# Optimization experiments

Measured on AMD Instinct MI355X. Metric: run time of the kernel, lower is better.

The kernel has to match this reference:

```python
import jax, jax.numpy as jnp
import numpy as np

NEG_SLOPE = 0.2
N_NODES = 51200      # batch 256 graphs x 200 nodes
NODE_PER_G = 200
IN_DIM = 200
HID = 64
HEADS = 4
N_CLASSES = 2
E_RAND = 16 * N_NODES


def setup_inputs() -> dict:
    key = jax.random.key(0)
    ks = jax.random.split(key, 12)
    feat = jax.random.normal(ks[0], (N_NODES, IN_DIM), dtype=jnp.float32)
    # random edges kept within each 200-node graph block + self-loops (no zero in-degree)
    g_off = (jnp.arange(E_RAND) % (N_NODES // NODE_PER_G)) * NODE_PER_G
    src = jax.random.randint(ks[1], (E_RAND,), 0, NODE_PER_G) + g_off
    dst = jax.random.randint(ks[2], (E_RAND,), 0, NODE_PER_G) + g_off
    loop = jnp.arange(N_NODES)
    src = jnp.concatenate([src, loop]).astype(jnp.int32)
    dst = jnp.concatenate([dst, loop]).astype(jnp.int32)
    s = 0.05
    W0 = jax.random.normal(ks[3], (IN_DIM, HEADS * HID), dtype=jnp.float32) * s
    al0 = jax.random.normal(ks[4], (HEADS, HID), dtype=jnp.float32) * s
    ar0 = jax.random.normal(ks[5], (HEADS, HID), dtype=jnp.float32) * s
    W1 = jax.random.normal(ks[6], (HEADS * HID, HEADS * HID), dtype=jnp.float32) * s
    al1 = jax.random.normal(ks[7], (HEADS, HID), dtype=jnp.float32) * s
    ar1 = jax.random.normal(ks[8], (HEADS, HID), dtype=jnp.float32) * s
    Wc = jax.random.normal(ks[9], (NODE_PER_G * HID, N_CLASSES), dtype=jnp.float32) * s
    bc = jnp.zeros((N_CLASSES,), dtype=jnp.float32)
    return {"feat": feat, "src": src, "dst": dst, "W0": W0, "al0": al0, "ar0": ar0,
            "W1": W1, "al1": al1, "ar1": ar1, "Wc": Wc, "bc": bc, "batch_size": 256}


def gat_conv(h, src, dst, W, al, ar, residual):
    N = h.shape[0]
    ft = (h @ W).reshape(N, HEADS, HID)                      # [N,H,D]
    el = jnp.einsum('nhd,hd->nh', ft, al)                    # [N,H]
    er = jnp.einsum('nhd,hd->nh', ft, ar)
    e = jax.nn.leaky_relu(el[src] + er[dst], NEG_SLOPE)      # [E,H]
    emax = jax.ops.segment_max(e, dst, num_segments=N)
    a = jnp.exp(e - emax[dst])
    denom = jax.ops.segment_sum(a, dst, num_segments=N)
    alpha = a / denom[dst]                                   # [E,H]
    out = jax.ops.segment_sum(alpha[:, :, None] * ft[src], dst, num_segments=N)
    if residual:
        out = out + h.reshape(N, HEADS, HID)                 # identity residual (in==H*D)
    return jax.nn.elu(out)                                   # [N,H,D]


def reference(feat, src, dst, W0, al0, ar0, W1, al1, ar1, Wc, bc, batch_size):
    h = gat_conv(feat, src, dst, W0, al0, ar0, residual=False)
    h = h.reshape(h.shape[0], HEADS * HID)                   # flatten(1)
    h = gat_conv(h, src, dst, W1, al1, ar1, residual=True)
    h = h.mean(axis=1)                                       # mean over heads -> [N,D]
    h = h.reshape(batch_size, -1)                            # [B, node*D]
    return h @ Wc + bc
```

## Files before the change

### kernel.cpp

```cpp
#include <hip/hip_runtime.h>
#include <hip/hip_bf16.h>
#include <hip/hip_fp16.h>

#define N_NODES_C   51200
#define NODE_PER_G  200
#define NGRAPH      256
#define HEADS       4
#define HID         64
#define FDIM        256
#define IN_DIM_C    200
#define E_RAND_C    819200
#define RAND_PER_G  3200
#define AWS         3208
#define NEG_SLOPE   0.2f

typedef _Float16 f16x8 __attribute__((ext_vector_type(8)));
typedef float    f32x4 __attribute__((ext_vector_type(4)));

__device__ __forceinline__ float leaky(float x) { return fmaxf(x, NEG_SLOPE * x); }

__global__ __launch_bounds__(1024) void build_csr(
    const int* __restrict__ src, const int* __restrict__ dst,
    uchar2* __restrict__ egs, int* __restrict__ goff,
    const float* __restrict__ W0, const float* __restrict__ W1,
    _Float16* __restrict__ W0t, _Float16* __restrict__ W1t)
{
    __shared__ uchar2 s_e[RAND_PER_G];
    __shared__ int s_cnt[256];
    __shared__ int s_off[256];

    const int g = blockIdx.x, tid = threadIdx.x;
    const int node0 = g * NODE_PER_G;
    uchar2* egsp = egs + (size_t)g * RAND_PER_G;

    {
        int idx = g * 1024 + tid;
        if (idx < (IN_DIM_C + FDIM) * FDIM) {
            int k = idx >> 8, n = idx & 255;
            if (k < IN_DIM_C)
                W0t[(size_t)n * IN_DIM_C + k] = (_Float16)W0[(size_t)k * FDIM + n];
            else {
                int kk = k - IN_DIM_C;
                W1t[(size_t)n * FDIM + kk] = (_Float16)W1[(size_t)kk * FDIM + n];
            }
        }
    }

    if (tid < 256) s_cnt[tid] = 0;
    __syncthreads();
    for (int e = tid; e < RAND_PER_G; e += 1024) {
        int eid = g + (e << 8);
        uchar2 ed = make_uchar2((unsigned char)(src[eid] - node0),
                                (unsigned char)(dst[eid] - node0));
        s_e[e] = ed;
        atomicAdd(&s_cnt[ed.y], 1);
    }
    __syncthreads();
    if (tid < 64) {
        const int base = tid << 2;
        int c0_ = s_cnt[base], c1 = s_cnt[base + 1];
        int c2 = s_cnt[base + 2], c3 = s_cnt[base + 3];
        s_cnt[base] = 0; s_cnt[base + 1] = 0;
        s_cnt[base + 2] = 0; s_cnt[base + 3] = 0;
        int s1 = c0_ + c1, s2 = s1 + c2, s3 = s2 + c3;
        int pre = s3;
#pragma unroll
        for (int d = 1; d < 64; d <<= 1) {
            int t = __shfl_up(pre, d);
            if (tid >= d) pre += t;
        }
        int excl = pre - s3;
        s_off[base]     = excl;
        s_off[base + 1] = excl + c0_;
        s_off[base + 2] = excl + s1;
        s_off[base + 3] = excl + s2;
    }
    __syncthreads();
    for (int e = tid; e < RAND_PER_G; e += 1024) {
        uchar2 ed = s_e[e];
        int pos = s_off[ed.y] + atomicAdd(&s_cnt[ed.y], 1);
        egsp[pos] = ed;
    }
    if (tid <= NODE_PER_G)
        goff[(size_t)g * 201 + tid] = s_off[tid];
}

__device__ __forceinline__ int swzoff(int m, int kg) {
    int pair = m >> 1;
    int slot = (((m & 1) << 2) | kg) ^ (pair & 7);
    return pair * 64 + slot * 8;
}

__device__ __forceinline__ f16x8 cvt8(float4 a, float4 b) {
    f16x8 r;
    r[0] = (_Float16)a.x; r[1] = (_Float16)a.y;
    r[2] = (_Float16)a.z; r[3] = (_Float16)a.w;
    r[4] = (_Float16)b.x; r[5] = (_Float16)b.y;
    r[6] = (_Float16)b.z; r[7] = (_Float16)b.w;
    return r;
}

template <bool L1>
__global__ __launch_bounds__(1024) void fused_gat(
    const void* __restrict__ A_, const _Float16* __restrict__ Bt, int K,
    const uchar2* __restrict__ egs, const int* __restrict__ goff,
    const float* __restrict__ al, const float* __restrict__ ar,
    const _Float16* __restrict__ hprev, const float* __restrict__ Wc,
    const float* __restrict__ bc, void* __restrict__ out_)
{
    __shared__ __align__(16) _Float16 s_ft[NODE_PER_G * FDIM];
    __shared__ __align__(16) unsigned s_aw[HEADS * AWS];
    __shared__ float s_el[NODE_PER_G * HEADS];
    __shared__ float s_er[NODE_PER_G * HEADS];
    __shared__ int   s_off[NODE_PER_G + 1];
    __shared__ float s_red[2];

    const int g = blockIdx.x, tid = threadIdx.x;
    const int node0 = g * NODE_PER_G;
    const int wave = tid >> 6, lane = tid & 63;
    const uchar2* egp = egs + (size_t)g * RAND_PER_G;

    if (tid < 2) s_red[tid] = 0.f;
    if (tid <= NODE_PER_G) s_off[tid] = goff[(size_t)g * 201 + tid];

    {
        _Float16* sA = (_Float16*)s_aw;
        _Float16* sB = (_Float16*)s_aw + 208 * 32;
        const int arow = tid >> 2;
        const int agk  = tid & 3;
        const int KC = (K + 31) >> 5;
        const int aoffL = swzoff(lane & 15, lane >> 4);
        const uint4 z4 = make_uint4(0u, 0u, 0u, 0u);

        f32x4 acc[4][4];
#pragma unroll
        for (int t = 0; t < 4; ++t)
#pragma unroll
            for (int ni = 0; ni < 4; ++ni) acc[t][ni] = (f32x4){0.f, 0.f, 0.f, 0.f};

        uint4  aR = z4, bR = z4;
        float4 ax = make_float4(0.f, 0.f, 0.f, 0.f), ay = ax;

        auto fetch = [&](int kc) {
            const int k8 = kc * 32 + agk * 8;
            if constexpr (L1) {
                const _Float16* A = (const _Float16*)A_;
                aR = (arow < NODE_PER_G && k8 + 8 <= K)
                    ? *(const uint4*)&A[(size_t)(node0 + arow) * K + k8] : z4;
            } else {
                const float* A = (const float*)A_;
                ax = make_float4(0.f, 0.f, 0.f, 0.f); ay = ax;
                if (arow < NODE_PER_G && k8 + 8 <= K) {
                    const float* pa = &A[(size_t)(node0 + arow) * K + k8];
                    ax = *(const float4*)pa;
                    ay = *(const float4*)(pa + 4);
                }
            }
            bR = (k8 + 8 <= K)
                ? *(const uint4*)&Bt[(size_t)arow * K + k8] : z4;
        };

        fetch(0);
        for (int kc = 0; kc < KC; ++kc) {
            __syncthreads();
            if (arow < 208) {
                if constexpr (L1) *(uint4*)&sA[swzoff(arow, agk)] = aR;
                else              *(f16x8*)&sA[swzoff(arow, agk)] = cvt8(ax, ay);
            }
            *(uint4*)&sB[swzoff(arow, agk)] = bR;
            __syncthreads();
            if (kc + 1 < KC) fetch(kc + 1);
#pragma unroll
            for (int t = 0; t < 4; ++t) {
                const int task = wave * 4 + t;
                if (task < 52) {
                    const int m16 = task >> 2, n64 = task & 3;
                    f16x8 af = *(const f16x8*)&sA[aoffL + m16 * 512];
#pragma unroll
                    for (int ni = 0; ni < 4; ++ni) {
                        f16x8 bf = *(const f16x8*)&sB[aoffL + n64 * 2048 + ni * 512];
                        acc[t][ni] = __builtin_amdgcn_mfma_f32_16x16x32_f16(
                            af, bf, acc[t][ni], 0, 0, 0);
                    }
                }
            }
        }
        __syncthreads();
        const int c = lane & 15;
#pragma unroll
        for (int t = 0; t < 4; ++t) {
            const int task = wave * 4 + t;
            if (task < 52) {
                const int m16 = task >> 2, n64 = task & 3;
                const int r0 = m16 * 16 + ((lane >> 4) << 2);
                const int cc = n64 * 64 + c;
                float alv[4], arv[4];
#pragma unroll
                for (int ni = 0; ni < 4; ++ni) {
                    alv[ni] = al[n64 * 64 + ni * 16 + c];
                    arv[ni] = ar[n64 * 64 + ni * 16 + c];
                }
#pragma unroll
                for (int r = 0; r < 4; ++r) {
                    const int row = r0 + r;
                    float e_l = 0.f, e_r = 0.f;
#pragma unroll
                    for (int ni = 0; ni < 4; ++ni) {
                        float v = acc[t][ni][r];
                        e_l = fmaf(v, alv[ni], e_l);
                        e_r = fmaf(v, arv[ni], e_r);
                        if (row < NODE_PER_G)
                            s_ft[row * FDIM + cc + ni * 16] = (_Float16)v;
                    }
#pragma unroll
                    for (int m = 1; m < 16; m <<= 1) {
                        e_l += __shfl_xor(e_l, m);
                        e_r += __shfl_xor(e_r, m);
                    }
                    if (c == 0 && row < NODE_PER_G) {
                        s_el[row * 4 + n64] = e_l;
                        s_er[row * 4 + n64] = e_r;
                    }
                }
            }
        }
    }
    __syncthreads();

    for (int e = tid; e < RAND_PER_G; e += 1024) {
        uchar2 ed = egp[e];
        float4 elv = *(const float4*)&s_el[ed.x * 4];
        float4 erv = *(const float4*)&s_er[ed.y * 4];
        unsigned sb = (unsigned)ed.x << 16;
        __half h0 = __float2half_rn(__expf(leaky(elv.x + erv.x)));
        __half h1 = __float2half_rn(__expf(leaky(elv.y + erv.y)));
        __half h2 = __float2half_rn(__expf(leaky(elv.z + erv.z)));
        __half h3 = __float2half_rn(__expf(leaky(elv.w + erv.w)));
        s_aw[e]           = sb | (unsigned)__half_as_ushort(h0);
        s_aw[AWS + e]     = sb | (unsigned)__half_as_ushort(h1);
        s_aw[2 * AWS + e] = sb | (unsigned)__half_as_ushort(h2);
        s_aw[3 * AWS + e] = sb | (unsigned)__half_as_ushort(h3);
    }
    __syncthreads();

    const int half = lane >> 5;
    const int l32 = lane & 31;
    const int c0 = l32 * 8;
    const int hh = l32 >> 3;
    const unsigned* awp = s_aw + hh * AWS;
    const __half hz = __ushort_as_half((unsigned short)0);
    const __half2 hz2 = __half2half2(hz);
    float w0 = 0.f, w1 = 0.f;

    for (int p = wave; p < NODE_PER_G / 2; p += 16) {
        const int n = half ? (p + 100) : p;
        const int begA = s_off[p],       lenA = s_off[p + 1] - begA;
        const int begB = s_off[p + 100], lenB = s_off[p + 101] - begB;
        const int beg = half ? begB : begA;
        const int len = half ? lenB : lenA;
        const int jmax = max(lenA, lenB);

        float a_self = __expf(leaky(s_el[n * 4 + hh] + s_er[n * 4 + hh]));
        __half as0 = __float2half_rn(a_self), as1 = hz;
        __half2 accA[4], accB[4], accC[4], accD[4];
        {
            uint4 v = *(const uint4*)&s_ft[n * FDIM + c0];
            const __half2* hv = (const __half2*)&v;
            __half2 as2 = __half2half2(as0);
#pragma unroll
            for (int q = 0; q < 4; ++q) {
                accA[q] = __hmul2(as2, hv[q]);
                accB[q] = hz2; accC[q] = hz2; accD[q] = hz2;
            }
        }

        int j = 0;
        for (; j + 4 <= jmax; j += 4) {
            unsigned wd0 = awp[(j     < len) ? (beg + j)     : 0];
            unsigned wd1 = awp[(j + 1 < len) ? (beg + j + 1) : 0];
            unsigned wd2 = awp[(j + 2 < len) ? (beg + j + 2) : 0];
            unsigned wd3 = awp[(j + 3 < len) ? (beg + j + 3) : 0];
            __half a0 = (j     < len) ? __ushort_as_half((unsigned short)wd0) : hz;
            __half a1 = (j + 1 < len) ? __ushort_as_half((unsigned short)wd1) : hz;
            __half a2 = (j + 2 < len) ? __ushort_as_half((unsigned short)wd2) : hz;
            __half a3 = (j + 3 < len) ? __ushort_as_half((unsigned short)wd3) : hz;
            uint4 v0 = *(const uint4*)&s_ft[(int)(wd0 >> 16) * FDIM + c0];
            uint4 v1 = *(const uint4*)&s_ft[(int)(wd1 >> 16) * FDIM + c0];
            uint4 v2 = *(const uint4*)&s_ft[(int)(wd2 >> 16) * FDIM + c0];
            uint4 v3 = *(const uint4*)&s_ft[(int)(wd3 >> 16) * FDIM + c0];
            as0 = __hadd(as0, __hadd(a0, a2));
            as1 = __hadd(as1, __hadd(a1, a3));
            __half2 a02 = __half2half2(a0), a12 = __half2half2(a1);
            __half2 a22 = __half2half2(a2), a32 = __half2half2(a3);
            const __half2* h0v = (const __half2*)&v0;
            const __half2* h1v = (const __half2*)&v1;
            const __half2* h2v = (const __half2*)&v2;
            const __half2* h3v = (const __half2*)&v3;
#pragma unroll
            for (int q = 0; q < 4; ++q) {
                accA[q] = __hfma2(a02, h0v[q], accA[q]);
                accB[q] = __hfma2(a12, h1v[q], accB[q]);
                accC[q] = __hfma2(a22, h2v[q], accC[q]);
                accD[q] = __hfma2(a32, h3v[q], accD[q]);
            }
        }
        for (; j < jmax; ++j) {
            unsigned wd0 = awp[(j < len) ? (beg + j) : 0];
            __half a0 = (j < len) ? __ushort_as_half((unsigned short)wd0) : hz;
            uint4 v0 = *(const uint4*)&s_ft[(int)(wd0 >> 16) * FDIM + c0];
            as0 = __hadd(as0, a0);
            __half2 a02 = __half2half2(a0);
            const __half2* h0v = (const __half2*)&v0;
#pragma unroll
            for (int q = 0; q < 4; ++q)
                accA[q] = __hfma2(a02, h0v[q], accA[q]);
        }

        float acc[8];
#pragma unroll
        for (int q = 0; q < 4; ++q) {
            __half2 s = __hadd2(__hadd2(accA[q], accB[q]),
                                __hadd2(accC[q], accD[q]));
            float2 f = __half22float2(s);
            acc[2 * q] = f.x;
            acc[2 * q + 1] = f.y;
        }
        const float rd = 1.f / __half2float(__hadd(as0, as1));
#pragma unroll
        for (int q = 0; q < 8; ++q) acc[q] *= rd;

        if constexpr (L1) {
            uint4 rv = *(const uint4*)&hprev[(size_t)(node0 + n) * FDIM + c0];
            const __half2* hv = (const __half2*)&rv;
#pragma unroll
            for (int q = 0; q < 4; ++q) {
                float2 f = __half22float2(hv[q]);
                acc[2 * q]     += f.x;
                acc[2 * q + 1] += f.y;
            }
#pragma unroll
            for (int q = 0; q < 8; ++q)
                acc[q] = (acc[q] > 0.f) ? acc[q] : expm1f(acc[q]);
#pragma unroll
            for (int q = 0; q < 8; ++q) {
                acc[q] += __shfl_xor(acc[q], 8);
                acc[q] += __shfl_xor(acc[q], 16);
            }
            if (l32 < 8) {
                const int d0 = l32 * 8;
                const float* wp = &Wc[((size_t)n * HID + d0) * 2];
#pragma unroll
                for (int q = 0; q < 8; ++q) {
                    float m = acc[q] * 0.25f;
                    w0 += m * wp[2 * q];
                    w1 += m * wp[2 * q + 1];
                }
            }
        } else {
#pragma unroll
            for (int q = 0; q < 8; ++q)
                acc[q] = (acc[q] > 0.f) ? acc[q] : expm1f(acc[q]);
            __half2 o[4];
#pragma unroll
            for (int q = 0; q < 4; ++q) {
                o[q].x = __float2half_rn(acc[2 * q]);
                o[q].y = __float2half_rn(acc[2 * q + 1]);
            }
            _Float16* outp = (_Float16*)out_;
            *(uint4*)&outp[(size_t)(node0 + n) * FDIM + c0] = *(uint4*)o;
        }
    }

    if constexpr (L1) {
#pragma unroll
        for (int m = 32; m >= 1; m >>= 1) {
            w0 += __shfl_xor(w0, m);
            w1 += __shfl_xor(w1, m);
        }
        if (lane == 0) {
            atomicAdd(&s_red[0], w0);
            atomicAdd(&s_red[1], w1);
        }
        __syncthreads();
        if (tid < 2) ((float*)out_)[g * 2 + tid] = s_red[tid] + bc[tid];
    }
}

extern "C" void kernel_launch(void* const* d_in, const int* in_sizes, int n_in,
                              void* d_out, int out_size, void* d_ws, size_t ws_size,
                              hipStream_t stream) {
    const float* feat = (const float*)d_in[0];
    const int*   src  = (const int*)d_in[1];
    const int*   dst  = (const int*)d_in[2];
    const float* W0   = (const float*)d_in[3];
    const float* al0  = (const float*)d_in[4];
    const float* ar0  = (const float*)d_in[5];
    const float* W1   = (const float*)d_in[6];
    const float* al1  = (const float*)d_in[7];
    const float* ar1  = (const float*)d_in[8];
    const float* Wc   = (const float*)d_in[9];
    const float* bc   = (const float*)d_in[10];
    float* out = (float*)d_out;

    _Float16* h0  = (_Float16*)d_ws;
    _Float16* W0t = h0 + (size_t)N_NODES_C * FDIM;
    _Float16* W1t = W0t + (size_t)FDIM * IN_DIM_C;
    uchar2*   egs = (uchar2*)(W1t + (size_t)FDIM * FDIM);
    int*      goff = (int*)(egs + (size_t)NGRAPH * RAND_PER_G);

    build_csr<<<NGRAPH, 1024, 0, stream>>>(src, dst, egs, goff, W0, W1, W0t, W1t);

    fused_gat<false><<<NGRAPH, 1024, 0, stream>>>(
        feat, W0t, IN_DIM_C, egs, goff, al0, ar0, nullptr, nullptr, nullptr, h0);

    fused_gat<true><<<NGRAPH, 1024, 0, stream>>>(
        h0, W1t, FDIM, egs, goff, al1, ar1, h0, Wc, bc, out);
}
```

Before: 112.2 us.

## Fuse both GAT layers into one per-graph kernel keeping layer-0 output on-chip

Merges the two per-layer kernels into a single kernel per graph. The layer-0 ELU output stays in registers (hres) and is written back into shared memory in a swizzled MFMA A-operand layout, where the layer-1 GEMM reads it directly. Only W1 is streamed from global memory. This removes the global round trip of the 51200x256 fp16 intermediate, one kernel launch, and the re-read of the residual input. The cost is a larger shared-memory footprint (~161KB), more live registers at 1024 threads/block, and the removal of the inter-layer launch boundary.

```diff
diff --git a/kernel.cpp b/kernel.cpp
--- a/kernel.cpp
+++ b/kernel.cpp
@@ -100,92 +100,46 @@
     return r;
 }
 
-template <bool L1>
-__global__ __launch_bounds__(1024) void fused_gat(
-    const void* __restrict__ A_, const _Float16* __restrict__ Bt, int K,
-    const uchar2* __restrict__ egs, const int* __restrict__ goff,
-    const float* __restrict__ al, const float* __restrict__ ar,
-    const _Float16* __restrict__ hprev, const float* __restrict__ Wc,
-    const float* __restrict__ bc, void* __restrict__ out_)
+__global__ __launch_bounds__(1024) void gat2(
+    const float* __restrict__ feat, const _Float16* __restrict__ W0t,
+    const _Float16* __restrict__ W1t, const uchar2* __restrict__ egs,
+    const int* __restrict__ goff,
+    const float* __restrict__ al0, const float* __restrict__ ar0,
+    const float* __restrict__ al1, const float* __restrict__ ar1,
+    const float* __restrict__ Wc, const float* __restrict__ bc,
+    float* __restrict__ out)
 {
-    __shared__ __align__(16) _Float16 s_ft[NODE_PER_G * FDIM];
-    __shared__ __align__(16) unsigned s_aw[HEADS * AWS];
-    __shared__ float s_el[NODE_PER_G * HEADS];
-    __shared__ float s_er[NODE_PER_G * HEADS];
-    __shared__ int   s_off[NODE_PER_G + 1];
-    __shared__ float s_red[2];
+    __shared__ __align__(16) char smem[160944];
+    _Float16* s_ft = (_Float16*)smem;
+    unsigned* s_aw = (unsigned*)(smem + 102400);
+    float*    s_el = (float*)(smem + 153728);
+    float*    s_er = (float*)(smem + 156928);
+    int*      s_off = (int*)(smem + 160128);
+    float*    s_red = (float*)(smem + 160936);
 
     const int g = blockIdx.x, tid = threadIdx.x;
     const int node0 = g * NODE_PER_G;
     const int wave = tid >> 6, lane = tid & 63;
     const uchar2* egp = egs + (size_t)g * RAND_PER_G;
 
+    const int arow = tid >> 2, agk = tid & 3;
+    const int aoffL = swzoff(lane & 15, lane >> 4);
+    const uint4 z4 = make_uint4(0u, 0u, 0u, 0u);
+    const int half = lane >> 5;
+    const int l32 = lane & 31;
+    const int cagg = l32 * 8;
+    const int hh = l32 >> 3;
+    const __half hz = __ushort_as_half((unsigned short)0);
+    const __half2 hz2 = __half2half2(hz);
+
+    __half2 hres[7][4];
+
     if (tid < 2) s_red[tid] = 0.f;
     if (tid <= NODE_PER_G) s_off[tid] = goff[(size_t)g * 201 + tid];
 
-    {
-        _Float16* sA = (_Float16*)s_aw;
-        _Float16* sB = (_Float16*)s_aw + 208 * 32;
-        const int arow = tid >> 2;
-        const int agk  = tid & 3;
-        const int KC = (K + 31) >> 5;
-        const int aoffL = swzoff(lane & 15, lane >> 4);
-        const uint4 z4 = make_uint4(0u, 0u, 0u, 0u);
-
-        f32x4 acc[4][4];
-#pragma unroll
-        for (int t = 0; t < 4; ++t)
-#pragma unroll
-            for (int ni = 0; ni < 4; ++ni) acc[t][ni] = (f32x4){0.f, 0.f, 0.f, 0.f};
-
-        uint4  aR = z4, bR = z4;
-        float4 ax = make_float4(0.f, 0.f, 0.f, 0.f), ay = ax;
-
-        auto fetch = [&](int kc) {
-            const int k8 = kc * 32 + agk * 8;
-            if constexpr (L1) {
-                const _Float16* A = (const _Float16*)A_;
-                aR = (arow < NODE_PER_G && k8 + 8 <= K)
-                    ? *(const uint4*)&A[(size_t)(node0 + arow) * K + k8] : z4;
-            } else {
-                const float* A = (const float*)A_;
-                ax = make_float4(0.f, 0.f, 0.f, 0.f); ay = ax;
-                if (arow < NODE_PER_G && k8 + 8 <= K) {
-                    const float* pa = &A[(size_t)(node0 + arow) * K + k8];
-                    ax = *(const float4*)pa;
-                    ay = *(const float4*)(pa + 4);
-                }
-            }
-            bR = (k8 + 8 <= K)
-                ? *(const uint4*)&Bt[(size_t)arow * K + k8] : z4;
-        };
-
-        fetch(0);
-        for (int kc = 0; kc < KC; ++kc) {
-            __syncthreads();
-            if (arow < 208) {
-                if constexpr (L1) *(uint4*)&sA[swzoff(arow, agk)] = aR;
-                else              *(f16x8*)&sA[swzoff(arow, agk)] = cvt8(ax, ay);
-            }
-            *(uint4*)&sB[swzoff(arow, agk)] = bR;
-            __syncthreads();
-            if (kc + 1 < KC) fetch(kc + 1);
-#pragma unroll
-            for (int t = 0; t < 4; ++t) {
-                const int task = wave * 4 + t;
-                if (task < 52) {
-                    const int m16 = task >> 2, n64 = task & 3;
-                    f16x8 af = *(const f16x8*)&sA[aoffL + m16 * 512];
-#pragma unroll
-                    for (int ni = 0; ni < 4; ++ni) {
-                        f16x8 bf = *(const f16x8*)&sB[aoffL + n64 * 2048 + ni * 512];
-                        acc[t][ni] = __builtin_amdgcn_mfma_f32_16x16x32_f16(
-                            af, bf, acc[t][ni], 0, 0, 0);
-                    }
-                }
-            }
-        }
-        __syncthreads();
+    f32x4 acc[4][4];
+
+    auto epilogue = [&](const float* alp, const float* arp) {
         const int c = lane & 15;
 #pragma unroll
         for (int t = 0; t < 4; ++t) {
@@ -197,8 +151,8 @@
                 float alv[4], arv[4];
 #pragma unroll
                 for (int ni = 0; ni < 4; ++ni) {
-                    alv[ni] = al[n64 * 64 + ni * 16 + c];
-                    arv[ni] = ar[n64 * 64 + ni * 16 + c];
+                    alv[ni] = alp[n64 * 64 + ni * 16 + c];
+                    arv[ni] = arp[n64 * 64 + ni * 16 + c];
                 }
 #pragma unroll
                 for (int r = 0; r < 4; ++r) {
@@ -224,47 +178,32 @@
                 }
             }
         }
-    }
-    __syncthreads();
-
-    for (int e = tid; e < RAND_PER_G; e += 1024) {
-        uchar2 ed = egp[e];
-        float4 elv = *(const float4*)&s_el[ed.x * 4];
-        float4 erv = *(const float4*)&s_er[ed.y * 4];
-        unsigned sb = (unsigned)ed.x << 16;
-        __half h0 = __float2half_rn(__expf(leaky(elv.x + erv.x)));
-        __half h1 = __float2half_rn(__expf(leaky(elv.y + erv.y)));
-        __half h2 = __float2half_rn(__expf(leaky(elv.z + erv.z)));
-        __half h3 = __float2half_rn(__expf(leaky(elv.w + erv.w)));
-        s_aw[e]           = sb | (unsigned)__half_as_ushort(h0);
-        s_aw[AWS + e]     = sb | (unsigned)__half_as_ushort(h1);
-        s_aw[2 * AWS + e] = sb | (unsigned)__half_as_ushort(h2);
-        s_aw[3 * AWS + e] = sb | (unsigned)__half_as_ushort(h3);
-    }
-    __syncthreads();
-
-    const int half = lane >> 5;
-    const int l32 = lane & 31;
-    const int c0 = l32 * 8;
-    const int hh = l32 >> 3;
-    const unsigned* awp = s_aw + hh * AWS;
-    const __half hz = __ushort_as_half((unsigned short)0);
-    const __half2 hz2 = __half2half2(hz);
-    float w0 = 0.f, w1 = 0.f;
-
-    for (int p = wave; p < NODE_PER_G / 2; p += 16) {
-        const int n = half ? (p + 100) : p;
-        const int begA = s_off[p],       lenA = s_off[p + 1] - begA;
-        const int begB = s_off[p + 100], lenB = s_off[p + 101] - begB;
-        const int beg = half ? begB : begA;
-        const int len = half ? lenB : lenA;
-        const int jmax = max(lenA, lenB);
-
+    };
+
+    auto alpha_fill = [&]() {
+        for (int e = tid; e < RAND_PER_G; e += 1024) {
+            uchar2 ed = egp[e];
+            float4 elv = *(const float4*)&s_el[ed.x * 4];
+            float4 erv = *(const float4*)&s_er[ed.y * 4];
+            unsigned sb = (unsigned)ed.x << 16;
+            __half h0 = __float2half_rn(__expf(leaky(elv.x + erv.x)));
+            __half h1 = __float2half_rn(__expf(leaky(elv.y + erv.y)));
+            __half h2 = __float2half_rn(__expf(leaky(elv.z + erv.z)));
+            __half h3 = __float2half_rn(__expf(leaky(elv.w + erv.w)));
+            s_aw[e]           = sb | (unsigned)__half_as_ushort(h0);
+            s_aw[AWS + e]     = sb | (unsigned)__half_as_ushort(h1);
+            s_aw[2 * AWS + e] = sb | (unsigned)__half_as_ushort(h2);
+            s_aw[3 * AWS + e] = sb | (unsigned)__half_as_ushort(h3);
+        }
+    };
+
+    auto agg_node = [&](int n, int beg, int len, int jmax, float* acc8) {
+        const unsigned* awp = s_aw + hh * AWS;
         float a_self = __expf(leaky(s_el[n * 4 + hh] + s_er[n * 4 + hh]));
         __half as0 = __float2half_rn(a_self), as1 = hz;
         __half2 accA[4], accB[4], accC[4], accD[4];
         {
-            uint4 v = *(const uint4*)&s_ft[n * FDIM + c0];
+            uint4 v = *(const uint4*)&s_ft[n * FDIM + cagg];
             const __half2* hv = (const __half2*)&v;
             __half2 as2 = __half2half2(as0);
 #pragma unroll
@@ -273,7 +212,6 @@
                 accB[q] = hz2; accC[q] = hz2; accD[q] = hz2;
             }
         }
-
         int j = 0;
         for (; j + 4 <= jmax; j += 4) {
             unsigned wd0 = awp[(j     < len) ? (beg + j)     : 0];
@@ -284,10 +222,10 @@
             __half a1 = (j + 1 < len) ? __ushort_as_half((unsigned short)wd1) : hz;
             __half a2 = (j + 2 < len) ? __ushort_as_half((unsigned short)wd2) : hz;
             __half a3 = (j + 3 < len) ? __ushort_as_half((unsigned short)wd3) : hz;
-            uint4 v0 = *(const uint4*)&s_ft[(int)(wd0 >> 16) * FDIM + c0];
-            uint4 v1 = *(const uint4*)&s_ft[(int)(wd1 >> 16) * FDIM + c0];
-            uint4 v2 = *(const uint4*)&s_ft[(int)(wd2 >> 16) * FDIM + c0];
-            uint4 v3 = *(const uint4*)&s_ft[(int)(wd3 >> 16) * FDIM + c0];
+            uint4 v0 = *(const uint4*)&s_ft[(int)(wd0 >> 16) * FDIM + cagg];
+            uint4 v1 = *(const uint4*)&s_ft[(int)(wd1 >> 16) * FDIM + cagg];
+            uint4 v2 = *(const uint4*)&s_ft[(int)(wd2 >> 16) * FDIM + cagg];
+            uint4 v3 = *(const uint4*)&s_ft[(int)(wd3 >> 16) * FDIM + cagg];
             as0 = __hadd(as0, __hadd(a0, a2));
             as1 = __hadd(as1, __hadd(a1, a3));
             __half2 a02 = __half2half2(a0), a12 = __half2half2(a1);
@@ -307,7 +245,7 @@
         for (; j < jmax; ++j) {
             unsigned wd0 = awp[(j < len) ? (beg + j) : 0];
             __half a0 = (j < len) ? __ushort_as_half((unsigned short)wd0) : hz;
-            uint4 v0 = *(const uint4*)&s_ft[(int)(wd0 >> 16) * FDIM + c0];
+            uint4 v0 = *(const uint4*)&s_ft[(int)(wd0 >> 16) * FDIM + cagg];
             as0 = __hadd(as0, a0);
             __half2 a02 = __half2half2(a0);
             const __half2* h0v = (const __half2*)&v0;
@@ -315,75 +253,195 @@
             for (int q = 0; q < 4; ++q)
                 accA[q] = __hfma2(a02, h0v[q], accA[q]);
         }
-
-        float acc[8];
+        const float rd = 1.f / __half2float(__hadd(as0, as1));
 #pragma unroll
         for (int q = 0; q < 4; ++q) {
             __half2 s = __hadd2(__hadd2(accA[q], accB[q]),
                                 __hadd2(accC[q], accD[q]));
             float2 f = __half22float2(s);
-            acc[2 * q] = f.x;
-            acc[2 * q + 1] = f.y;
-        }
-        const float rd = 1.f / __half2float(__hadd(as0, as1));
-#pragma unroll
-        for (int q = 0; q < 8; ++q) acc[q] *= rd;
-
-        if constexpr (L1) {
-            uint4 rv = *(const uint4*)&hprev[(size_t)(node0 + n) * FDIM + c0];
-            const __half2* hv = (const __half2*)&rv;
+            acc8[2 * q]     = f.x * rd;
+            acc8[2 * q + 1] = f.y * rd;
+        }
+    };
+
+    {
+        _Float16* sA = (_Float16*)s_aw;
+        _Float16* sB = (_Float16*)s_aw + 208 * 32;
+        const int KC = 7;
+#pragma unroll
+        for (int t = 0; t < 4; ++t)
+#pragma unroll
+            for (int ni = 0; ni < 4; ++ni) acc[t][ni] = (f32x4){0.f, 0.f, 0.f, 0.f};
+
+        float4 ax = make_float4(0.f, 0.f, 0.f, 0.f), ay = ax;
+        uint4 bR = z4;
+        auto fetch0 = [&](int kc) {
+            const int k8 = kc * 32 + agk * 8;
+            ax = make_float4(0.f, 0.f, 0.f, 0.f); ay = ax;
+            if (arow < NODE_PER_G && k8 + 8 <= IN_DIM_C) {
+                const float* pa = &feat[(size_t)(node0 + arow) * IN_DIM_C + k8];
+                ax = *(const float4*)pa;
+                ay = *(const float4*)(pa + 4);
+            }
+            bR = (k8 + 8 <= IN_DIM_C)
+                ? *(const uint4*)&W0t[(size_t)arow * IN_DIM_C + k8] : z4;
+        };
+        fetch0(0);
+        for (int kc = 0; kc < KC; ++kc) {
+            __syncthreads();
+            if (arow < 208) *(f16x8*)&sA[swzoff(arow, agk)] = cvt8(ax, ay);
+            *(uint4*)&sB[swzoff(arow, agk)] = bR;
+            __syncthreads();
+            if (kc + 1 < KC) fetch0(kc + 1);
+#pragma unroll
+            for (int t = 0; t < 4; ++t) {
+                const int task = wave * 4 + t;
+                if (task < 52) {
+                    const int m16 = task >> 2, n64 = task & 3;
+                    f16x8 af = *(const f16x8*)&sA[aoffL + m16 * 512];
+#pragma unroll
+                    for (int ni = 0; ni < 4; ++ni) {
+                        f16x8 bf = *(const f16x8*)&sB[aoffL + n64 * 2048 + ni * 512];
+                        acc[t][ni] = __builtin_amdgcn_mfma_f32_16x16x32_f16(
+                            af, bf, acc[t][ni], 0, 0, 0);
+                    }
+                }
+            }
+        }
+        __syncthreads();
+        epilogue(al0, ar0);
+    }
+    __syncthreads();
+
+    alpha_fill();
+    __syncthreads();
+#pragma unroll
+    for (int i = 0; i < 7; ++i) {
+        const int p = wave + 16 * i;
+        if (p < NODE_PER_G / 2) {
+            const int n = half ? (p + 100) : p;
+            const int begA = s_off[p],       lenA = s_off[p + 1] - begA;
+            const int begB = s_off[p + 100], lenB = s_off[p + 101] - begB;
+            const int beg = half ? begB : begA;
+            const int len = half ? lenB : lenA;
+            const int jmax = max(lenA, lenB);
+            float a8[8];
+            agg_node(n, beg, len, jmax, a8);
+#pragma unroll
+            for (int q = 0; q < 8; ++q)
+                a8[q] = (a8[q] > 0.f) ? a8[q] : expm1f(a8[q]);
 #pragma unroll
             for (int q = 0; q < 4; ++q) {
-                float2 f = __half22float2(hv[q]);
-                acc[2 * q]     += f.x;
-                acc[2 * q + 1] += f.y;
+                __half2 h;
+                h.x = __float2half_rn(a8[2 * q]);
+                h.y = __float2half_rn(a8[2 * q + 1]);
+                hres[i][q] = h;
+            }
+        } else {
+#pragma unroll
+            for (int q = 0; q < 4; ++q) hres[i][q] = hz2;
+        }
+    }
+    __syncthreads();
+
+#pragma unroll
+    for (int i = 0; i < 7; ++i) {
+        const int p = wave + 16 * i;
+        if (p < NODE_PER_G / 2) {
+            const int n = half ? (p + 100) : p;
+            *(uint4*)&s_ft[(cagg >> 5) * 6400 + swzoff(n, (cagg & 31) >> 3)] =
+                *(uint4*)hres[i];
+        }
+    }
+    __syncthreads();
+
+    {
+        _Float16* sB = (_Float16*)s_aw;
+#pragma unroll
+        for (int t = 0; t < 4; ++t)
+#pragma unroll
+            for (int ni = 0; ni < 4; ++ni) acc[t][ni] = (f32x4){0.f, 0.f, 0.f, 0.f};
+
+        uint4 bR = *(const uint4*)&W1t[(size_t)arow * FDIM + agk * 8];
+        for (int kc = 0; kc < 8; ++kc) {
+            __syncthreads();
+            *(uint4*)&sB[swzoff(arow, agk)] = bR;
+            __syncthreads();
+            if (kc + 1 < 8)
+                bR = *(const uint4*)&W1t[(size_t)arow * FDIM + (kc + 1) * 32 + agk * 8];
+            const int cbase = kc * 6400;
+#pragma unroll
+            for (int t = 0; t < 4; ++t) {
+                const int task = wave * 4 + t;
+                if (task < 52) {
+                    const int m16 = task >> 2, n64 = task & 3;
+                    f16x8 af = *(const f16x8*)&s_ft[cbase + aoffL + m16 * 512];
+#pragma unroll
+                    for (int ni = 0; ni < 4; ++ni) {
+                        f16x8 bf = *(const f16x8*)&sB[aoffL + n64 * 2048 + ni * 512];
+                        acc[t][ni] = __builtin_amdgcn_mfma_f32_16x16x32_f16(
+                            af, bf, acc[t][ni], 0, 0, 0);
+                    }
+                }
+            }
+        }
+        __syncthreads();
+        epilogue(al1, ar1);
+    }
+    __syncthreads();
+
+    alpha_fill();
+    __syncthreads();
+    float w0 = 0.f, w1 = 0.f;
+#pragma unroll
+    for (int i = 0; i < 7; ++i) {
+        const int p = wave + 16 * i;
+        if (p < NODE_PER_G / 2) {
+            const int n = half ? (p + 100) : p;
+            const int begA = s_off[p],       lenA = s_off[p + 1] - begA;
+            const int begB = s_off[p + 100], lenB = s_off[p + 101] - begB;
+            const int beg = half ? begB : begA;
+            const int len = half ? lenB : lenA;
+            const int jmax = max(lenA, lenB);
+            float a8[8];
+            agg_node(n, beg, len, jmax, a8);
+#pragma unroll
+            for (int q = 0; q < 4; ++q) {
+                float2 r = __half22float2(hres[i][q]);
+                a8[2 * q]     += r.x;
+                a8[2 * q + 1] += r.y;
             }
 #pragma unroll
             for (int q = 0; q < 8; ++q)
-                acc[q] = (acc[q] > 0.f) ? acc[q] : expm1f(acc[q]);
+                a8[q] = (a8[q] > 0.f) ? a8[q] : expm1f(a8[q]);
 #pragma unroll
             for (int q = 0; q < 8; ++q) {
-                acc[q] += __shfl_xor(acc[q], 8);
-                acc[q] += __shfl_xor(acc[q], 16);
+                a8[q] += __shfl_xor(a8[q], 8);
+                a8[q] += __shfl_xor(a8[q], 16);
             }
             if (l32 < 8) {
                 const int d0 = l32 * 8;
                 const float* wp = &Wc[((size_t)n * HID + d0) * 2];
 #pragma unroll
                 for (int q = 0; q < 8; ++q) {
-                    float m = acc[q] * 0.25f;
+                    float m = a8[q] * 0.25f;
                     w0 += m * wp[2 * q];
                     w1 += m * wp[2 * q + 1];
                 }
             }
-        } else {
-#pragma unroll
-            for (int q = 0; q < 8; ++q)
-                acc[q] = (acc[q] > 0.f) ? acc[q] : expm1f(acc[q]);
-            __half2 o[4];
-#pragma unroll
-            for (int q = 0; q < 4; ++q) {
-                o[q].x = __float2half_rn(acc[2 * q]);
-                o[q].y = __float2half_rn(acc[2 * q + 1]);
-            }
-            _Float16* outp = (_Float16*)out_;
-            *(uint4*)&outp[(size_t)(node0 + n) * FDIM + c0] = *(uint4*)o;
-        }
-    }
-
-    if constexpr (L1) {
-#pragma unroll
-        for (int m = 32; m >= 1; m >>= 1) {
-            w0 += __shfl_xor(w0, m);
-            w1 += __shfl_xor(w1, m);
-        }
-        if (lane == 0) {
-            atomicAdd(&s_red[0], w0);
-            atomicAdd(&s_red[1], w1);
-        }
-        __syncthreads();
-        if (tid < 2) ((float*)out_)[g * 2 + tid] = s_red[tid] + bc[tid];
-    }
+        }
+    }
+#pragma unroll
+    for (int m = 32; m >= 1; m >>= 1) {
+        w0 += __shfl_xor(w0, m);
+        w1 += __shfl_xor(w1, m);
+    }
+    if (lane == 0) {
+        atomicAdd(&s_red[0], w0);
+        atomicAdd(&s_red[1], w1);
+    }
+    __syncthreads();
+    if (tid < 2) out[g * 2 + tid] = s_red[tid] + bc[tid];
 }
 
 extern "C" void kernel_launch(void* const* d_in, const int* in_sizes, int n_in,
@@ -402,17 +460,13 @@
     const float* bc   = (const float*)d_in[10];
     float* out = (float*)d_out;
 
-    _Float16* h0  = (_Float16*)d_ws;
-    _Float16* W0t = h0 + (size_t)N_NODES_C * FDIM;
+    _Float16* W0t = (_Float16*)d_ws;
     _Float16* W1t = W0t + (size_t)FDIM * IN_DIM_C;
     uchar2*   egs = (uchar2*)(W1t + (size_t)FDIM * FDIM);
     int*      goff = (int*)(egs + (size_t)NGRAPH * RAND_PER_G);
 
     build_csr<<<NGRAPH, 1024, 0, stream>>>(src, dst, egs, goff, W0, W1, W0t, W1t);
 
-    fused_gat<false><<<NGRAPH, 1024, 0, stream>>>(
-        feat, W0t, IN_DIM_C, egs, goff, al0, ar0, nullptr, nullptr, nullptr, h0);
-
-    fused_gat<true><<<NGRAPH, 1024, 0, stream>>>(
-        h0, W1t, FDIM, egs, goff, al1, ar1, h0, Wc, bc, out);
+    gat2<<<NGRAPH, 1024, 0, stream>>>(feat, W0t, W1t, egs, goff,
+                                      al0, ar0, al1, ar1, Wc, bc, out);
 }
```

After: 117.3 us. 1.05x slower.
